# Kernel optimization log

Hardware: AMD Instinct MI355X
Metric: run time of the kernel (lower is better)

## Reference

```python
import jax, jax.numpy as jnp
import numpy as np

CONF_THR = 0.5   # hard-coded `confidence` in pre_process_pred
NMS_THR = 0.5    # hard-coded `nms_conf` in pre_process_pred
IMG = 608.0


def setup_inputs() -> dict:
    key = jax.random.key(0)
    k1, k2, k3 = jax.random.split(key, 3)
    B, N, C = 16, 2048, 80
    u = jax.random.uniform(k1, (B, N, 4), dtype=jnp.float32)
    # cx, cy in [0, 608); w, h in [2, 120) pixels (YOLO-style pixel coords, matches +1 IoU convention)
    pred_boxes = jnp.concatenate([u[..., :2] * IMG, 2.0 + u[..., 2:] * 118.0], axis=-1)
    pred_objectness = jax.random.uniform(k2, (B, N, 1), dtype=jnp.float32)
    pred_logits = jax.random.uniform(k3, (B, N, C), dtype=jnp.float32)
    return {"pred_boxes": pred_boxes, "pred_objectness": pred_objectness, "pred_logits": pred_logits}


def _pairwise_iou(b):
    # b: [N,4] xyxy; +1 pixel convention exactly as original bbox_iou
    x1 = jnp.maximum(b[:, None, 0], b[None, :, 0])
    y1 = jnp.maximum(b[:, None, 1], b[None, :, 1])
    x2 = jnp.minimum(b[:, None, 2], b[None, :, 2])
    y2 = jnp.minimum(b[:, None, 3], b[None, :, 3])
    inter = jnp.clip(x2 - x1 + 1.0, 0.0) * jnp.clip(y2 - y1 + 1.0, 0.0)
    area = (b[:, 2] - b[:, 0] + 1.0) * (b[:, 3] - b[:, 1] + 1.0)
    return inter / (area[:, None] + area[None, :] - inter)


def _nms_one(boxes, obj, logits):
    # boxes: [N,4] cxcywh, obj: [N], logits: [N,C]
    N = boxes.shape[0]
    cx, cy, w, h = boxes[:, 0], boxes[:, 1], boxes[:, 2], boxes[:, 3]
    xyxy = jnp.stack([cx - w / 2, cy - h / 2, cx + w / 2, cy + h / 2], axis=-1)
    valid = obj > CONF_THR                    # confidence gate (strict >, as in original)
    cls_conf = jnp.max(logits, axis=-1)       # max_conf
    cls = jnp.argmax(logits, axis=-1)         # max_conf_score (class index)
    # sort by objectness descending; invalid boxes pushed to the end
    score = jnp.where(valid, obj, -jnp.inf)
    order = jnp.argsort(-score)
    xyxy_s = xyxy[order]
    obj_s = obj[order]
    valid_s = valid[order]
    cls_s = cls[order]
    conf_s = cls_conf[order]
    iou = _pairwise_iou(jax.lax.stop_gradient(xyxy_s))   # [N,N]
    same = cls_s[:, None] == cls_s[None, :]              # per-class NMS grouping
    idx = jnp.arange(N)

    def body(i, alive):
        # a box suppresses only if it is itself still alive & valid (greedy removal semantics)
        sup = alive[i] & valid_s[i] & (iou[i] >= NMS_THR) & same[i] & (idx > i)
        return alive & ~sup

    alive = jax.lax.fori_loop(0, N, body, valid_s)
    keep = alive & valid_s
    det = jnp.concatenate(
        [xyxy_s, obj_s[:, None], conf_s[:, None], cls_s.astype(xyxy_s.dtype)[:, None]], axis=-1
    )  # [N,7] = (x1,y1,x2,y2,obj,cls_conf,cls)
    return jnp.where(keep[:, None], det, 0.0)


def reference(pred_boxes, pred_objectness, pred_logits):
    obj = pred_objectness[..., 0]
    dets = jax.vmap(_nms_one)(pred_boxes, obj, pred_logits)  # [B,N,7]
    B, N, _ = dets.shape
    bind = jnp.broadcast_to(jnp.arange(B, dtype=dets.dtype)[:, None, None], (B, N, 1))
    # [B,N,8]: (batch_ind, x1,y1,x2,y2, obj, cls_conf, cls); suppressed rows are all-zero padding
    return jnp.concatenate([bind, dets], axis=-1)
```

## Files before the change

kernel.cpp:

```cpp
#include <hip/hip_runtime.h>
#include <stdint.h>

#define BB 16
#define NN 2048
#define CC 80
#define CONF_THRV 0.5f
#define NMS_THRV 0.5f

__global__ void k_classify(const float* __restrict__ logits,
                           const float* __restrict__ obj,
                           float* __restrict__ conf0,
                           int* __restrict__ cls0,
                           unsigned long long* __restrict__ keys) {
  int idx = blockIdx.x * blockDim.x + threadIdx.x;
  if (idx >= BB * NN) return;
  const float4* lp = (const float4*)(logits + (size_t)idx * CC);
  float best = -INFINITY;
  int bi = 0;
  #pragma unroll
  for (int q = 0; q < CC / 4; ++q) {
    float4 v = lp[q];
    if (v.x > best) { best = v.x; bi = 4 * q + 0; }
    if (v.y > best) { best = v.y; bi = 4 * q + 1; }
    if (v.z > best) { best = v.z; bi = 4 * q + 2; }
    if (v.w > best) { best = v.w; bi = 4 * q + 3; }
  }
  conf0[idx] = best;
  cls0[idx] = bi;
  float o = obj[idx];
  float s = (o > CONF_THRV) ? o : -INFINITY;
  unsigned u = __float_as_uint(s);
  u = (u & 0x80000000u) ? ~u : (u | 0x80000000u);
  unsigned n = (unsigned)(idx & (NN - 1));
  keys[idx] = ((unsigned long long)u << 32) | (unsigned long long)(0xFFFFFFFFu - n);
}

__global__ __launch_bounds__(256) void k_rank_scatter(
    const float4* __restrict__ boxes,
    const float* __restrict__ obj,
    const unsigned long long* __restrict__ keys,
    const float* __restrict__ conf0,
    const int* __restrict__ cls0,
    float4* __restrict__ sxyxy,
    float* __restrict__ sarea,
    float* __restrict__ sobj,
    float* __restrict__ sconf,
    int* __restrict__ scls,
    int* __restrict__ nvalid) {
  __shared__ unsigned long long lk[NN];
  int b = blockIdx.y;
  int t = threadIdx.x;
  size_t base = (size_t)b * NN;
  #pragma unroll
  for (int r = 0; r < NN / 256; ++r)
    lk[t + r * 256] = keys[base + t + r * 256];
  __syncthreads();

  int i = blockIdx.x * 256 + t;
  unsigned long long ki = lk[i];
  const unsigned long long VK = (0xBF000000ull << 32) | 0xFFFFFFFFull;
  int rank = 0, vcnt = 0;
  const ulonglong2* lk2 = (const ulonglong2*)lk;
  #pragma unroll 4
  for (int j = 0; j < NN / 2; j += 2) {
    ulonglong2 a = lk2[j];
    ulonglong2 c = lk2[j + 1];
    rank += (a.x > ki) + (a.y > ki) + (c.x > ki) + (c.y > ki);
    vcnt += (a.x > VK) + (a.y > VK) + (c.x > VK) + (c.y > VK);
  }
  if (t == 0) nvalid[b] = vcnt;

  float4 bx = boxes[base + i];
  float hw = bx.z / 2.0f, hh = bx.w / 2.0f;
  float x1 = bx.x - hw, y1 = bx.y - hh;
  float x2 = bx.x + hw, y2 = bx.y + hh;
  sxyxy[base + rank] = make_float4(x1, y1, x2, y2);
  sarea[base + rank] = __fmul_rn(x2 - x1 + 1.0f, y2 - y1 + 1.0f);
  sobj[base + rank] = obj[base + i];
  sconf[base + rank] = conf0[base + i];
  scls[base + rank] = cls0[base + i];
}

__global__ void k_masks(const float4* __restrict__ sxyxy,
                        const float* __restrict__ sarea,
                        const int* __restrict__ scls,
                        const int* __restrict__ nvalid,
                        uint32_t* __restrict__ masksT) {
  int b = blockIdx.y;
  int pair = blockIdx.x * blockDim.x + threadIdx.x;
  int i = pair & (NN - 1);
  int w = pair >> 11;
  int nv = nvalid[b];
  size_t base = (size_t)b * NN;
  uint32_t bits = 0;
  int j0 = w * 32;
  int jend = min(j0 + 32, nv);
  int jstart = max(j0, i + 1);
  if (i < nv && jstart < jend) {
    float4 bi = sxyxy[base + i];
    float ai = sarea[base + i];
    int ci = scls[base + i];
    for (int j = jstart; j < jend; ++j) {
      float4 bj = sxyxy[base + j];
      float xx1 = fmaxf(bi.x, bj.x);
      float yy1 = fmaxf(bi.y, bj.y);
      float xx2 = fminf(bi.z, bj.z);
      float yy2 = fminf(bi.w, bj.w);
      float cw = fmaxf(xx2 - xx1 + 1.0f, 0.0f);
      float ch = fmaxf(yy2 - yy1 + 1.0f, 0.0f);
      float inter = __fmul_rn(cw, ch);
      float aj = sarea[base + j];
      float denom = (ai + aj) - inter;
      float iou = inter / denom;
      if (iou >= NMS_THRV && scls[base + j] == ci) bits |= (1u << (j - j0));
    }
  }
  masksT[((size_t)b * 64 + w) * NN + i] = bits;
}

__global__ __launch_bounds__(512) void k_scan_write(
    const uint32_t* __restrict__ masksT,
    const int* __restrict__ nvalid,
    const float4* __restrict__ sxyxy,
    const float* __restrict__ sobj,
    const float* __restrict__ sconf,
    const int* __restrict__ scls,
    float* __restrict__ out) {
  __shared__ uint32_t rsh[64];
  int b = blockIdx.x;
  int t = threadIdx.x;

  if (t < 64) {
    int lane = t;
    const uint4* col = (const uint4*)(masksT + ((size_t)b * 64 + lane) * NN);
    uint32_t remv = 0;
    uint4 A[8], B[8], C[8], D[8];
#define LOADBUF(BUF, CH) do {                                          \
      _Pragma("unroll")                                                \
      for (int q = 0; q < 8; ++q) BUF[q] = col[(CH) * 8 + q];          \
    } while (0)
    LOADBUF(A, 0); LOADBUF(B, 1); LOADBUF(C, 2); LOADBUF(D, 3);
#define STEP(BUF, CH, RCH) do {                                        \
      uint32_t cur[32];                                                \
      _Pragma("unroll")                                                \
      for (int q = 0; q < 8; ++q) {                                    \
        cur[4*q+0] = BUF[q].x; cur[4*q+1] = BUF[q].y;                  \
        cur[4*q+2] = BUF[q].z; cur[4*q+3] = BUF[q].w;                  \
      }                                                                \
      { int rr = (RCH) < 64 ? (RCH) : 0; LOADBUF(BUF, rr); }           \
      uint32_t all_or = 0;                                             \
      _Pragma("unroll")                                                \
      for (int d = 0; d < 32; ++d) all_or |= cur[d];                   \
      uint32_t word_c = (uint32_t)__shfl((int)remv, (CH), 64);         \
      uint32_t diag   = (uint32_t)__shfl((int)all_or, (CH), 64);       \
      if (diag == 0u) {                                                \
        if (word_c == 0u) {                                            \
          remv |= all_or;                                              \
        } else {                                                       \
          uint32_t acc = 0;                                            \
          _Pragma("unroll")                                            \
          for (int d = 0; d < 32; ++d)                                 \
            acc |= ((word_c >> d) & 1u) ? 0u : cur[d];                 \
          remv |= acc;                                                 \
        }                                                              \
      } else {                                                         \
        uint32_t wc = word_c, acc = 0;                                 \
        _Pragma("unroll")                                              \
        for (int d = 0; d < 32; ++d) {                                 \
          uint32_t dd = (uint32_t)__shfl((int)cur[d], (CH), 64);       \
          if (((wc >> d) & 1u) == 0u) { wc |= dd; acc |= cur[d]; }     \
        }                                                              \
        remv |= acc;                                                   \
      }                                                                \
    } while (0)
    for (int c = 0; c < 64; c += 4) {
      STEP(A, c + 0, c + 4);
      STEP(B, c + 1, c + 5);
      STEP(C, c + 2, c + 6);
      STEP(D, c + 3, c + 7);
    }
#undef STEP
#undef LOADBUF
    rsh[lane] = remv;
  }
  __syncthreads();

  int nv = nvalid[b];
  #pragma unroll
  for (int rep = 0; rep < 4; ++rep) {
    int r = t + rep * 512;
    size_t idx = (size_t)b * NN + r;
    bool keep = false;
    if (r < nv) {
      uint32_t wrd = rsh[r >> 5];
      keep = !((wrd >> (r & 31)) & 1u);
    }
    float4 xy = make_float4(0.f, 0.f, 0.f, 0.f);
    float o = 0.f, cf = 0.f, cl = 0.f;
    if (keep) {
      xy = sxyxy[idx];
      o = sobj[idx];
      cf = sconf[idx];
      cl = (float)scls[idx];
    }
    float4* op = (float4*)(out + idx * 8);
    op[0] = make_float4((float)b, xy.x, xy.y, xy.z);
    op[1] = make_float4(xy.w, o, cf, cl);
  }
}

extern "C" void kernel_launch(void* const* d_in, const int* in_sizes, int n_in,
                              void* d_out, int out_size, void* d_ws, size_t ws_size,
                              hipStream_t stream) {
  const float4* boxes = (const float4*)d_in[0];
  const float* obj = (const float*)d_in[1];
  const float* logits = (const float*)d_in[2];
  float* out = (float*)d_out;

  char* ws = (char*)d_ws;
  size_t off = 0;
  float4* sxyxy = (float4*)(ws + off);            off += (size_t)BB * NN * 16;
  unsigned long long* keys = (unsigned long long*)(ws + off); off += (size_t)BB * NN * 8;
  float* conf0 = (float*)(ws + off);              off += (size_t)BB * NN * 4;
  int* cls0 = (int*)(ws + off);                   off += (size_t)BB * NN * 4;
  float* sarea = (float*)(ws + off);              off += (size_t)BB * NN * 4;
  float* sobj = (float*)(ws + off);               off += (size_t)BB * NN * 4;
  float* sconf = (float*)(ws + off);              off += (size_t)BB * NN * 4;
  int* scls = (int*)(ws + off);                   off += (size_t)BB * NN * 4;
  int* nvalid = (int*)(ws + off);                 off += 256;
  uint32_t* masksT = (uint32_t*)(ws + off);       off += (size_t)BB * NN * 64 * 4;

  hipLaunchKernelGGL(k_classify, dim3((BB * NN + 255) / 256), dim3(256), 0, stream,
                     logits, obj, conf0, cls0, keys);
  hipLaunchKernelGGL(k_rank_scatter, dim3(NN / 256, BB), dim3(256), 0, stream,
                     boxes, obj, keys, conf0, cls0,
                     sxyxy, sarea, sobj, sconf, scls, nvalid);
  hipLaunchKernelGGL(k_masks, dim3(NN * 64 / 256, BB), dim3(256), 0, stream,
                     sxyxy, sarea, scls, nvalid, masksT);
  hipLaunchKernelGGL(k_scan_write, dim3(BB), dim3(512), 0, stream,
                     masksT, nvalid, sxyxy, sobj, sconf, scls, out);
}
```

Before: 158.6 us.

## Fuse classify into rank kernel and skip work for invalid boxes

Merges the classify kernel into the rank/scatter kernel, so keys are built in shared memory and argmax over logits runs only for valid boxes. This drops a launch and the keys/conf/cls workspace round trips. Mask threads for word columns beyond the valid count exit early, and the scan loop runs only over the valid chunks. Masks past nwords are no longer written, which relies on the scan only reading active lanes.

Result: faster. 147.7 us (-6.9%).

```diff
diff --git a/kernel.cpp b/kernel.cpp
--- a/kernel.cpp
+++ b/kernel.cpp
@@ -7,40 +7,10 @@
 #define CONF_THRV 0.5f
 #define NMS_THRV 0.5f
 
-__global__ void k_classify(const float* __restrict__ logits,
-                           const float* __restrict__ obj,
-                           float* __restrict__ conf0,
-                           int* __restrict__ cls0,
-                           unsigned long long* __restrict__ keys) {
-  int idx = blockIdx.x * blockDim.x + threadIdx.x;
-  if (idx >= BB * NN) return;
-  const float4* lp = (const float4*)(logits + (size_t)idx * CC);
-  float best = -INFINITY;
-  int bi = 0;
-  #pragma unroll
-  for (int q = 0; q < CC / 4; ++q) {
-    float4 v = lp[q];
-    if (v.x > best) { best = v.x; bi = 4 * q + 0; }
-    if (v.y > best) { best = v.y; bi = 4 * q + 1; }
-    if (v.z > best) { best = v.z; bi = 4 * q + 2; }
-    if (v.w > best) { best = v.w; bi = 4 * q + 3; }
-  }
-  conf0[idx] = best;
-  cls0[idx] = bi;
-  float o = obj[idx];
-  float s = (o > CONF_THRV) ? o : -INFINITY;
-  unsigned u = __float_as_uint(s);
-  u = (u & 0x80000000u) ? ~u : (u | 0x80000000u);
-  unsigned n = (unsigned)(idx & (NN - 1));
-  keys[idx] = ((unsigned long long)u << 32) | (unsigned long long)(0xFFFFFFFFu - n);
-}
-
-__global__ __launch_bounds__(256) void k_rank_scatter(
+__global__ __launch_bounds__(256) void k_rank_all(
     const float4* __restrict__ boxes,
     const float* __restrict__ obj,
-    const unsigned long long* __restrict__ keys,
-    const float* __restrict__ conf0,
-    const int* __restrict__ cls0,
+    const float* __restrict__ logits,
     float4* __restrict__ sxyxy,
     float* __restrict__ sarea,
     float* __restrict__ sobj,
@@ -48,27 +18,54 @@
     int* __restrict__ scls,
     int* __restrict__ nvalid) {
   __shared__ unsigned long long lk[NN];
+  __shared__ int cnt;
   int b = blockIdx.y;
   int t = threadIdx.x;
+  if (t == 0) cnt = 0;
+  __syncthreads();
   size_t base = (size_t)b * NN;
+  int myv = 0;
   #pragma unroll
-  for (int r = 0; r < NN / 256; ++r)
-    lk[t + r * 256] = keys[base + t + r * 256];
+  for (int r = 0; r < NN / 256; ++r) {
+    int a = t + r * 256;
+    float o = obj[base + a];
+    bool v = o > CONF_THRV;
+    float s = v ? o : -INFINITY;
+    unsigned u = __float_as_uint(s);
+    u = (u & 0x80000000u) ? ~u : (u | 0x80000000u);
+    lk[a] = ((unsigned long long)u << 32) |
+            (unsigned long long)(0xFFFFFFFFu - (unsigned)a);
+    myv += v ? 1 : 0;
+  }
+  atomicAdd(&cnt, myv);
   __syncthreads();
+  if (t == 0) nvalid[b] = cnt;
 
   int i = blockIdx.x * 256 + t;
   unsigned long long ki = lk[i];
   const unsigned long long VK = (0xBF000000ull << 32) | 0xFFFFFFFFull;
-  int rank = 0, vcnt = 0;
+  if (ki <= VK) return;
+
+  int rank = 0;
   const ulonglong2* lk2 = (const ulonglong2*)lk;
   #pragma unroll 4
   for (int j = 0; j < NN / 2; j += 2) {
-    ulonglong2 a = lk2[j];
-    ulonglong2 c = lk2[j + 1];
-    rank += (a.x > ki) + (a.y > ki) + (c.x > ki) + (c.y > ki);
-    vcnt += (a.x > VK) + (a.y > VK) + (c.x > VK) + (c.y > VK);
-  }
-  if (t == 0) nvalid[b] = vcnt;
+    ulonglong2 a2 = lk2[j];
+    ulonglong2 c2 = lk2[j + 1];
+    rank += (a2.x > ki) + (a2.y > ki) + (c2.x > ki) + (c2.y > ki);
+  }
+
+  const float4* lp = (const float4*)(logits + (base + i) * CC);
+  float best = -INFINITY;
+  int bi = 0;
+  #pragma unroll
+  for (int q = 0; q < CC / 4; ++q) {
+    float4 v4 = lp[q];
+    if (v4.x > best) { best = v4.x; bi = 4 * q + 0; }
+    if (v4.y > best) { best = v4.y; bi = 4 * q + 1; }
+    if (v4.z > best) { best = v4.z; bi = 4 * q + 2; }
+    if (v4.w > best) { best = v4.w; bi = 4 * q + 3; }
+  }
 
   float4 bx = boxes[base + i];
   float hw = bx.z / 2.0f, hh = bx.w / 2.0f;
@@ -77,8 +74,8 @@
   sxyxy[base + rank] = make_float4(x1, y1, x2, y2);
   sarea[base + rank] = __fmul_rn(x2 - x1 + 1.0f, y2 - y1 + 1.0f);
   sobj[base + rank] = obj[base + i];
-  sconf[base + rank] = conf0[base + i];
-  scls[base + rank] = cls0[base + i];
+  sconf[base + rank] = best;
+  scls[base + rank] = bi;
 }
 
 __global__ void k_masks(const float4* __restrict__ sxyxy,
@@ -91,6 +88,8 @@
   int i = pair & (NN - 1);
   int w = pair >> 11;
   int nv = nvalid[b];
+  int nwords = (nv + 31) >> 5;
+  if (w >= nwords) return;
   size_t base = (size_t)b * NN;
   uint32_t bits = 0;
   int j0 = w * 32;
@@ -129,15 +128,25 @@
   __shared__ uint32_t rsh[64];
   int b = blockIdx.x;
   int t = threadIdx.x;
+  int nv = nvalid[b];
 
   if (t < 64) {
     int lane = t;
+    int nwords = (nv + 31) >> 5;
+    int nch4 = (nwords + 3) & ~3;
+    bool act = lane < nwords;
     const uint4* col = (const uint4*)(masksT + ((size_t)b * 64 + lane) * NN);
     uint32_t remv = 0;
+    uint4 z4; z4.x = z4.y = z4.z = z4.w = 0u;
     uint4 A[8], B[8], C[8], D[8];
+    #pragma unroll
+    for (int q = 0; q < 8; ++q) { A[q] = z4; B[q] = z4; C[q] = z4; D[q] = z4; }
 #define LOADBUF(BUF, CH) do {                                          \
-      _Pragma("unroll")                                                \
-      for (int q = 0; q < 8; ++q) BUF[q] = col[(CH) * 8 + q];          \
+      if (act) {                                                       \
+        int rr = (CH) < 64 ? (CH) : 0;                                 \
+        _Pragma("unroll")                                              \
+        for (int q = 0; q < 8; ++q) BUF[q] = col[rr * 8 + q];          \
+      }                                                                \
     } while (0)
     LOADBUF(A, 0); LOADBUF(B, 1); LOADBUF(C, 2); LOADBUF(D, 3);
 #define STEP(BUF, CH, RCH) do {                                        \
@@ -147,7 +156,7 @@
         cur[4*q+0] = BUF[q].x; cur[4*q+1] = BUF[q].y;                  \
         cur[4*q+2] = BUF[q].z; cur[4*q+3] = BUF[q].w;                  \
       }                                                                \
-      { int rr = (RCH) < 64 ? (RCH) : 0; LOADBUF(BUF, rr); }           \
+      LOADBUF(BUF, RCH);                                               \
       uint32_t all_or = 0;                                             \
       _Pragma("unroll")                                                \
       for (int d = 0; d < 32; ++d) all_or |= cur[d];                   \
@@ -173,7 +182,7 @@
         remv |= acc;                                                   \
       }                                                                \
     } while (0)
-    for (int c = 0; c < 64; c += 4) {
+    for (int c = 0; c < nch4; c += 4) {
       STEP(A, c + 0, c + 4);
       STEP(B, c + 1, c + 5);
       STEP(C, c + 2, c + 6);
@@ -185,7 +194,6 @@
   }
   __syncthreads();
 
-  int nv = nvalid[b];
   #pragma unroll
   for (int rep = 0; rep < 4; ++rep) {
     int r = t + rep * 512;
@@ -220,9 +228,6 @@
   char* ws = (char*)d_ws;
   size_t off = 0;
   float4* sxyxy = (float4*)(ws + off);            off += (size_t)BB * NN * 16;
-  unsigned long long* keys = (unsigned long long*)(ws + off); off += (size_t)BB * NN * 8;
-  float* conf0 = (float*)(ws + off);              off += (size_t)BB * NN * 4;
-  int* cls0 = (int*)(ws + off);                   off += (size_t)BB * NN * 4;
   float* sarea = (float*)(ws + off);              off += (size_t)BB * NN * 4;
   float* sobj = (float*)(ws + off);               off += (size_t)BB * NN * 4;
   float* sconf = (float*)(ws + off);              off += (size_t)BB * NN * 4;
@@ -230,10 +235,8 @@
   int* nvalid = (int*)(ws + off);                 off += 256;
   uint32_t* masksT = (uint32_t*)(ws + off);       off += (size_t)BB * NN * 64 * 4;
 
-  hipLaunchKernelGGL(k_classify, dim3((BB * NN + 255) / 256), dim3(256), 0, stream,
-                     logits, obj, conf0, cls0, keys);
-  hipLaunchKernelGGL(k_rank_scatter, dim3(NN / 256, BB), dim3(256), 0, stream,
-                     boxes, obj, keys, conf0, cls0,
+  hipLaunchKernelGGL(k_rank_all, dim3(NN / 256, BB), dim3(256), 0, stream,
+                     boxes, obj, logits,
                      sxyxy, sarea, sobj, sconf, scls, nvalid);
   hipLaunchKernelGGL(k_masks, dim3(NN * 64 / 256, BB), dim3(256), 0, stream,
                      sxyxy, sarea, scls, nvalid, masksT);
```
